# Performance work log

Measured on AMD Instinct MI355X. Metric: run time of the kernel, lower is better.

The kernel has to match this reference:

```python
import jax, jax.numpy as jnp
import numpy as np

IN_CH = 256
OUT_CH = 256
K = 3
STRIDE = 1
PAD = 1
NUM_EMB = 8


def setup_inputs() -> dict:
    key = jax.random.key(0)
    ks = jax.random.split(key, 6)
    B, H, W = 16, 64, 64
    x = jax.random.normal(ks[0], (B, IN_CH, H, W), dtype=jnp.float32)
    kernal_embed = jax.random.normal(ks[1], (NUM_EMB, IN_CH, OUT_CH, K, K), dtype=jnp.float32)
    # 1x1 conv params (stored as a dense [out,in] matrix) + bias
    cls_conv_w = jax.random.normal(ks[2], (IN_CH, IN_CH), dtype=jnp.float32) / np.sqrt(IN_CH)
    cls_conv_b = jax.random.normal(ks[3], (IN_CH,), dtype=jnp.float32) * 0.01
    cls_dense_w = jax.random.normal(ks[4], (NUM_EMB, IN_CH), dtype=jnp.float32) / np.sqrt(IN_CH)
    cls_dense_b = jax.random.normal(ks[5], (NUM_EMB,), dtype=jnp.float32) * 0.01
    return {"x": x, "kernal_embed": kernal_embed, "cls_conv_w": cls_conv_w,
            "cls_conv_b": cls_conv_b, "cls_dense_w": cls_dense_w, "cls_dense_b": cls_dense_b}


def reference(x, kernal_embed, cls_conv_w, cls_conv_b, cls_dense_w, cls_dense_b):
    B, C, H, W = x.shape
    # 1x1 conv -> global avg pool -> dense -> softmax weights over embeddings
    w = jnp.einsum('bchw,dc->bdhw', x, cls_conv_w) + cls_conv_b[None, :, None, None]
    pooled = jnp.mean(w, axis=(2, 3))                       # (B, C)
    logits = pooled @ cls_dense_w.T + cls_dense_b           # (B, E)
    mix = jax.nn.softmax(logits, axis=1)                    # (B, E)
    # Per-sample kernel synthesis: (B, in, out, k, k)
    kern = jnp.einsum('be,eiojk->biojk', mix, kernal_embed)
    # Faithful to torch .view(-1, in, k, k): raw reshape (mixes in/out axes as in original)
    kern = kern.reshape(B, OUT_CH, IN_CH, K, K)
    # Grouped conv with groups=B == per-sample conv via vmap
    def conv1(xi, wi):
        # xi: (C, H, W), wi: (out, in, k, k)
        return jax.lax.conv_general_dilated(
            xi[None], wi, window_strides=(STRIDE, STRIDE),
            padding=[(PAD, PAD), (PAD, PAD)],
            dimension_numbers=('NCHW', 'OIHW', 'NCHW'))[0]
    out = jax.vmap(conv1)(x, kern)                          # (B, out, H, W)
    return out
```

## Files before the change

kernel.cpp:

```cpp
#include <hip/hip_runtime.h>
#include <stdint.h>

#define B_  16
#define C_  256
#define H_  64
#define W_  64
#define P_  4096
#define E_  8
#define HP_ 66

typedef __bf16 bf16x8 __attribute__((ext_vector_type(8)));
typedef float  f32x4  __attribute__((ext_vector_type(4)));

__device__ __forceinline__ unsigned short f2bf(float f) {
    union { float f; unsigned int u; } v; v.f = f;
    unsigned int u = v.u;
    unsigned int r = (u + 0x7fffu + ((u >> 16) & 1u)) >> 16;
    return (unsigned short)r;
}

__device__ __forceinline__ void async_load16(const void* g, void* l) {
    __builtin_amdgcn_global_load_lds(
        (const __attribute__((address_space(1))) void*)g,
        (__attribute__((address_space(3))) void*)l, 16, 0, 0);
}

__global__ void k_xpose(const float* __restrict__ x, unsigned short* __restrict__ Xp,
                        float* __restrict__ xsum) {
    const int bid = blockIdx.x;
    const int tid = threadIdx.x;

    if (bid < 520) {
        const int gid = bid * 256 + tid;
        const int pix = gid >> 5;
        const int chunk = gid & 31;
        const int bb = pix / 260;
        const int j = pix - bb * 260;
        int h, w;
        if (j < 66)       { h = 0;  w = j; }
        else if (j < 132) { h = 65; w = j - 66; }
        else { int jj = j - 132; h = 1 + (jj & 63); w = (jj < 64) ? 0 : 65; }
        const uint4 z = {0u, 0u, 0u, 0u};
        *(uint4*)(Xp + ((size_t)((bb * HP_ + h) * HP_ + w) << 8) + chunk * 8) = z;
    }

    const int b  = bid >> 8;
    const int h  = (bid >> 2) & 63;
    const int cg = bid & 3;
    const int c0 = cg << 6;
    __shared__ float tile[64][65];
    {
        const int ci = tid >> 2, wseg = tid & 3;
        const float* src = x + ((size_t)(b * 256 + c0 + ci) << 12) + (h << 6) + wseg * 16;
        float s = 0.f;
#pragma unroll
        for (int i = 0; i < 4; ++i) {
            float4 v = *(const float4*)(src + i * 4);
            tile[ci][wseg * 16 + i * 4 + 0] = v.x;
            tile[ci][wseg * 16 + i * 4 + 1] = v.y;
            tile[ci][wseg * 16 + i * 4 + 2] = v.z;
            tile[ci][wseg * 16 + i * 4 + 3] = v.w;
            s += v.x + v.y + v.z + v.w;
        }
        s += __shfl_down(s, 1, 64);
        s += __shfl_down(s, 2, 64);
        if ((tid & 3) == 0) atomicAdd(&xsum[b * 256 + c0 + ci], s);
    }
    __syncthreads();
    {
        const int w = tid >> 2, cs = tid & 3;
        unsigned short ov[16] __attribute__((aligned(16)));
#pragma unroll
        for (int k = 0; k < 16; ++k) ov[k] = f2bf(tile[cs * 16 + k][w]);
        unsigned short* dst = Xp + ((size_t)((b * HP_ + h + 1) * HP_ + (w + 1)) << 8) + c0 + cs * 16;
        ((uint4*)dst)[0] = ((const uint4*)ov)[0];
        ((uint4*)dst)[1] = ((const uint4*)ov)[1];
    }
}

__global__ void k_mix(const float* __restrict__ xsum,
                      const float* __restrict__ cw, const float* __restrict__ cb,
                      const float* __restrict__ dw, const float* __restrict__ db,
                      float* __restrict__ mix) {
    const int b = blockIdx.x, tid = threadIdx.x;
    __shared__ __align__(16) float sxm[256];
    __shared__ __align__(16) float spool[256];
    __shared__ float sl[8];
    sxm[tid] = xsum[b * 256 + tid] * (1.0f / P_);
    __syncthreads();
    {
        float a = cb[tid];
        const float4* cwr = (const float4*)(cw + (size_t)tid * 256);
        const float4* xv4 = (const float4*)sxm;
#pragma unroll 8
        for (int c = 0; c < 64; ++c) {
            const float4 wv = cwr[c];
            const float4 xv = xv4[c];
            a += wv.x * xv.x + wv.y * xv.y + wv.z * xv.z + wv.w * xv.w;
        }
        spool[tid] = a;
    }
    __syncthreads();
    if (tid < 64) {
        const int e = tid >> 3, dl = tid & 7;
        float part = 0.f;
#pragma unroll 4
        for (int d = dl; d < 256; d += 8) part += dw[e * 256 + d] * spool[d];
        part += __shfl_down(part, 4, 64);
        part += __shfl_down(part, 2, 64);
        part += __shfl_down(part, 1, 64);
        if (dl == 0) sl[e] = part + db[e];
    }
    __syncthreads();
    if (tid < 8) {
        float m = sl[0];
        for (int e = 1; e < 8; ++e) m = fmaxf(m, sl[e]);
        float den = 0.f;
        for (int e = 0; e < 8; ++e) den += __expf(sl[e] - m);
        mix[b * 8 + tid] = __expf(sl[tid] - m) / den;
    }
}

__global__ void k_mixkern(const float* __restrict__ KE, const float* __restrict__ mix,
                          unsigned short* __restrict__ Wg) {
    const int o    = blockIdx.x >> 1;
    const int half = blockIdx.x & 1;
    const int ic0  = half << 7;
    const int tid  = threadIdx.x;
    __shared__ __align__(16) float s[8][1152];
    __shared__ float smix[128];
    if (tid < 128) smix[tid] = mix[tid];
#pragma unroll
    for (int e = 0; e < 8; ++e) {
        const float4* src = (const float4*)(KE + (size_t)(e * 256 + o) * 2304 + ic0 * 9);
        float4* dst = (float4*)s[e];
        dst[tid] = src[tid];
        if (tid < 32) dst[256 + tid] = src[256 + tid];
    }
    __syncthreads();
    const int icl = tid & 127;
    const int b0  = (tid >> 7) << 3;
#pragma unroll
    for (int t = 0; t < 9; ++t) {
        float v[8];
#pragma unroll
        for (int e = 0; e < 8; ++e) v[e] = s[e][icl * 9 + t];
#pragma unroll
        for (int bb = 0; bb < 8; ++bb) {
            const int b = b0 + bb;
            float acc = 0.f;
#pragma unroll
            for (int e = 0; e < 8; ++e) acc += smix[b * 8 + e] * v[e];
            Wg[((size_t)(b * 256 + o) * 9 + t) * 256 + ic0 + icl] = f2bf(acc);
        }
    }
}

__global__ __launch_bounds__(512, 2) void k_gemm(const unsigned short* __restrict__ Wg,
                                                 const unsigned short* __restrict__ Xp,
                                                 float* __restrict__ out) {
    __shared__ __align__(16) unsigned short L[4][16384];
    const int tid = threadIdx.x;
    const int bid = blockIdx.x;
    const int xcd = bid & 7;
    const int g   = bid >> 3;
    const int b   = xcd + ((g >> 4) << 3);
    const int tile = g & 15;
    const int h0  = tile << 2;

    const int wid  = tid >> 6;
    const int lane = tid & 63;
    const int wm   = wid >> 2;
    const int wn   = wid & 3;
    const int ql   = lane & 15;
    const int quad = lane >> 4;
    const int sw   = ql & 7;

    const int srow = tid >> 3;
    const int csrc = (tid & 7) ^ (srow & 7);

    f32x4 acc[8][4];
#pragma unroll
    for (int i = 0; i < 8; ++i)
#pragma unroll
        for (int j = 0; j < 4; ++j) acc[i][j] = (f32x4)0.0f;

    auto stageA = [&](int s, int P) {
        const int t = s >> 2, kc = s & 3;
        const unsigned short* ga = Wg + ((size_t)(b * 256 + srow) * 9 + t) * 256
                                   + kc * 64 + csrc * 8;
#pragma unroll
        for (int j = 0; j < 4; ++j)
            async_load16(ga + (size_t)j * 64 * 9 * 256, (char*)L[P] + tid * 16 + j * 8192);
    };
    auto stageB = [&](int s, int P) {
        const int t = s >> 2, kc = s & 3;
        const int kh = t / 3, kw = t - kh * 3;
#pragma unroll
        for (int j = 0; j < 4; ++j)
            async_load16(Xp + (((size_t)((b * HP_ + h0 + j + kh) * HP_ + (srow + kw))) << 8)
                             + kc * 64 + csrc * 8,
                         (char*)L[2 + P] + tid * 16 + j * 8192);
    };

    bf16x8 af0[4], af1[4], bv[4];

#define MPH(AP, BP, KK, PREF_STMT, VM_STMT)                                        \
    do {                                                                           \
        _Pragma("unroll")                                                          \
        for (int r_ = 0; r_ < 4; ++r_)                                             \
            af0[r_] = *(const bf16x8*)((const char*)L[AP]                          \
                      + (wm * 128 + r_ * 16 + ql) * 128                            \
                      + (((((KK) << 2) | quad) ^ sw) << 4));                       \
        _Pragma("unroll")                                                          \
        for (int r_ = 0; r_ < 4; ++r_)                                             \
            af1[r_] = *(const bf16x8*)((const char*)L[AP]                          \
                      + (wm * 128 + 64 + r_ * 16 + ql) * 128                       \
                      + (((((KK) << 2) | quad) ^ sw) << 4));                       \
        _Pragma("unroll")                                                          \
        for (int r_ = 0; r_ < 4; ++r_)                                             \
            bv[r_] = *(const bf16x8*)((const char*)L[BP]                           \
                     + (wn * 64 + r_ * 16 + ql) * 128                              \
                     + (((((KK) << 2) | quad) ^ sw) << 4));                        \
        PREF_STMT;                                                                 \
        VM_STMT;                                                                   \
        asm volatile("s_barrier" ::: "memory");                                    \
        asm volatile("s_waitcnt lgkmcnt(0)" ::: "memory");                         \
        __builtin_amdgcn_s_setprio(1);                                             \
        _Pragma("unroll")                                                          \
        for (int r_ = 0; r_ < 4; ++r_)                                             \
            _Pragma("unroll")                                                      \
            for (int n_ = 0; n_ < 4; ++n_)                                         \
                acc[r_][n_] = __builtin_amdgcn_mfma_f32_16x16x32_bf16(             \
                    af0[r_], bv[n_], acc[r_][n_], 0, 0, 0);                        \
        _Pragma("unroll")                                                          \
        for (int r_ = 0; r_ < 4; ++r_)                                             \
            _Pragma("unroll")                                                      \
            for (int n_ = 0; n_ < 4; ++n_)                                         \
                acc[4 + r_][n_] = __builtin_amdgcn_mfma_f32_16x16x32_bf16(         \
                    af1[r_], bv[n_], acc[4 + r_][n_], 0, 0, 0);                    \
        __builtin_amdgcn_s_setprio(0);                                             \
    } while (0)

    stageA(0, 0); stageB(0, 0);
    asm volatile("s_waitcnt vmcnt(0)" ::: "memory");
    asm volatile("s_barrier" ::: "memory");

    for (int i = 0; i < 18; ++i) {
        const int sE = 2 * i;
        const int sO = sE + 1;
        const bool pf = (i < 17);
        MPH(0, 2, 0, { stageA(sO, 1); stageB(sO, 1); }, ((void)0));
        MPH(0, 2, 1, ((void)0),
            { asm volatile("s_waitcnt vmcnt(0)" ::: "memory"); });
        MPH(1, 3, 0, if (pf) { stageA(sE + 2, 0); stageB(sE + 2, 0); }, ((void)0));
        MPH(1, 3, 1, ((void)0),
            if (pf) { asm volatile("s_waitcnt vmcnt(0)" ::: "memory"); });
    }
#undef MPH

#pragma unroll
    for (int m = 0; m < 8; ++m) {
        const int mh = m >> 2, mr = m & 3;
        const int o = wm * 128 + mh * 64 + mr * 16 + quad * 4;
#pragma unroll
        for (int n = 0; n < 4; ++n) {
            const int w = n * 16 + ql;
            float* po = out + ((size_t)(b * 256 + o) << 12) + ((h0 + wn) << 6) + w;
#pragma unroll
            for (int r = 0; r < 4; ++r) po[(size_t)r << 12] = acc[mh * 4 + mr][n][r];
        }
    }
}

extern "C" void kernel_launch(void* const* d_in, const int* in_sizes, int n_in,
                              void* d_out, int out_size, void* d_ws, size_t ws_size,
                              hipStream_t stream) {
    const float* x  = (const float*)d_in[0];
    const float* KE = (const float*)d_in[1];
    const float* cw = (const float*)d_in[2];
    const float* cb = (const float*)d_in[3];
    const float* dw = (const float*)d_in[4];
    const float* db = (const float*)d_in[5];
    float* out = (float*)d_out;

    char* ws = (char*)d_ws;
    float* xsum           = (float*)(ws + 0);
    float* mix            = (float*)(ws + 16384);
    unsigned short* Wg    = (unsigned short*)(ws + 32768);
    unsigned short* Xp    = (unsigned short*)(ws + 32768 + 18874368);

    hipMemsetAsync(xsum, 0, B_ * C_ * sizeof(float), stream);
    k_xpose  <<<dim3(B_ * H_ * 4),    dim3(256), 0, stream>>>(x, Xp, xsum);
    k_mix    <<<dim3(B_),             dim3(256), 0, stream>>>(xsum, cw, cb, dw, db, mix);
    k_mixkern<<<dim3(C_ * 2),         dim3(256), 0, stream>>>(KE, mix, Wg);
    k_gemm   <<<dim3(256),            dim3(512), 0, stream>>>(Wg, Xp, out);
}
```

Baseline: 246.4 us.

## Interleave LDS fragment reads with MFMA and drop per-phase barriers

Each K-stage is restructured from two phases, each reading all fragments, barrier-syncing, waiting on LDS and then running MFMAs, into one window that interleaves the LDS reads for the second k-slice with MFMAs on the first. It adds a second B fragment buffer (bvn) and relies on compiler-inserted waits instead of explicit lgkmcnt(0)/barrier per phase. It also removes s_setprio. This halves the barriers per stage and hides LDS latency behind matrix math, at the cost of more registers.

```diff
diff --git a/kernel.cpp b/kernel.cpp
--- a/kernel.cpp
+++ b/kernel.cpp
@@ -203,43 +203,39 @@
                          (char*)L[2 + P] + tid * 16 + j * 8192);
     };
 
-    bf16x8 af0[4], af1[4], bv[4];
-
-#define MPH(AP, BP, KK, PREF_STMT, VM_STMT)                                        \
+    bf16x8 af0[4], af1[4], bv[4], bvn[4];
+
+#define AFADDR(AP, ROW, KK) ((const bf16x8*)((const char*)L[AP]                    \
+        + (wm * 128 + (ROW) * 16 + ql) * 128 + (((((KK) << 2) | quad) ^ sw) << 4)))
+#define BVADDR(BP, ROW, KK) ((const bf16x8*)((const char*)L[BP]                    \
+        + (wn * 64 + (ROW) * 16 + ql) * 128 + (((((KK) << 2) | quad) ^ sw) << 4)))
+
+#define RD_AF0(AP, KK) { _Pragma("unroll") for (int r_ = 0; r_ < 4; ++r_) af0[r_] = *AFADDR(AP, r_, KK); }
+#define RD_AF1(AP, KK) { _Pragma("unroll") for (int r_ = 0; r_ < 4; ++r_) af1[r_] = *AFADDR(AP, 4 + r_, KK); }
+#define RD_BV(BP, KK)  { _Pragma("unroll") for (int r_ = 0; r_ < 4; ++r_) bv[r_]  = *BVADDR(BP, r_, KK); }
+#define RD_BVN(BP, KK) { _Pragma("unroll") for (int r_ = 0; r_ < 4; ++r_) bvn[r_] = *BVADDR(BP, r_, KK); }
+
+#define MF16(AF, BB, MBASE)                                                        \
+    { _Pragma("unroll")                                                            \
+      for (int r_ = 0; r_ < 4; ++r_)                                               \
+          _Pragma("unroll")                                                        \
+          for (int n_ = 0; n_ < 4; ++n_)                                           \
+              acc[(MBASE) + r_][n_] = __builtin_amdgcn_mfma_f32_16x16x32_bf16(     \
+                  AF[r_], BB[n_], acc[(MBASE) + r_][n_], 0, 0, 0); }
+
+#define WINDOW(AP, BP, PREF_STMT, VM_STMT)                                         \
     do {                                                                           \
-        _Pragma("unroll")                                                          \
-        for (int r_ = 0; r_ < 4; ++r_)                                             \
-            af0[r_] = *(const bf16x8*)((const char*)L[AP]                          \
-                      + (wm * 128 + r_ * 16 + ql) * 128                            \
-                      + (((((KK) << 2) | quad) ^ sw) << 4));                       \
-        _Pragma("unroll")                                                          \
-        for (int r_ = 0; r_ < 4; ++r_)                                             \
-            af1[r_] = *(const bf16x8*)((const char*)L[AP]                          \
-                      + (wm * 128 + 64 + r_ * 16 + ql) * 128                       \
-                      + (((((KK) << 2) | quad) ^ sw) << 4));                       \
-        _Pragma("unroll")                                                          \
-        for (int r_ = 0; r_ < 4; ++r_)                                             \
-            bv[r_] = *(const bf16x8*)((const char*)L[BP]                           \
-                     + (wn * 64 + r_ * 16 + ql) * 128                              \
-                     + (((((KK) << 2) | quad) ^ sw) << 4));                        \
-        PREF_STMT;                                                                 \
+        RD_AF0(AP, 0); RD_AF1(AP, 0); RD_BV(BP, 0);             \
+        PREF_STMT;                                             \
+        MF16(af0, bv, 0);                                  \
+        RD_AF0(AP, 1);                                             \
+        RD_BVN(BP, 1);                                             \
+        MF16(af1, bv, 4);                               \
+        RD_AF1(AP, 1);                                             \
+        MF16(af0, bvn, 0);                                        \
+        MF16(af1, bvn, 4);                                        \
         VM_STMT;                                                                   \
         asm volatile("s_barrier" ::: "memory");                                    \
-        asm volatile("s_waitcnt lgkmcnt(0)" ::: "memory");                         \
-        __builtin_amdgcn_s_setprio(1);                                             \
-        _Pragma("unroll")                                                          \
-        for (int r_ = 0; r_ < 4; ++r_)                                             \
-            _Pragma("unroll")                                                      \
-            for (int n_ = 0; n_ < 4; ++n_)                                         \
-                acc[r_][n_] = __builtin_amdgcn_mfma_f32_16x16x32_bf16(             \
-                    af0[r_], bv[n_], acc[r_][n_], 0, 0, 0);                        \
-        _Pragma("unroll")                                                          \
-        for (int r_ = 0; r_ < 4; ++r_)                                             \
-            _Pragma("unroll")                                                      \
-            for (int n_ = 0; n_ < 4; ++n_)                                         \
-                acc[4 + r_][n_] = __builtin_amdgcn_mfma_f32_16x16x32_bf16(         \
-                    af1[r_], bv[n_], acc[4 + r_][n_], 0, 0, 0);                    \
-        __builtin_amdgcn_s_setprio(0);                                             \
     } while (0)
 
     stageA(0, 0); stageB(0, 0);
@@ -250,14 +246,21 @@
         const int sE = 2 * i;
         const int sO = sE + 1;
         const bool pf = (i < 17);
-        MPH(0, 2, 0, { stageA(sO, 1); stageB(sO, 1); }, ((void)0));
-        MPH(0, 2, 1, ((void)0),
-            { asm volatile("s_waitcnt vmcnt(0)" ::: "memory"); });
-        MPH(1, 3, 0, if (pf) { stageA(sE + 2, 0); stageB(sE + 2, 0); }, ((void)0));
-        MPH(1, 3, 1, ((void)0),
-            if (pf) { asm volatile("s_waitcnt vmcnt(0)" ::: "memory"); });
-    }
-#undef MPH
+        WINDOW(0, 2,
+               { stageA(sO, 1); stageB(sO, 1); },
+               { asm volatile("s_waitcnt vmcnt(0)" ::: "memory"); });
+        WINDOW(1, 3,
+               if (pf) { stageA(sE + 2, 0); stageB(sE + 2, 0); },
+               if (pf) { asm volatile("s_waitcnt vmcnt(0)" ::: "memory"); });
+    }
+#undef WINDOW
+#undef MF16
+#undef RD_AF0
+#undef RD_AF1
+#undef RD_BV
+#undef RD_BVN
+#undef AFADDR
+#undef BVADDR
 
 #pragma unroll
     for (int m = 0; m < 8; ++m) {
```

Result: no change. 246.4 us (+0.0%).
